# Performance work log

Hardware: AMD Instinct MI355X
Metric: run time of the kernel (lower is better)

Reference implementation:

```python
import jax, jax.numpy as jnp
import numpy as np

T, B_SZ = 1024, 1024
NX, NU, ND, NM, NDT, NH = 128, 64, 32, 32, 32, 128


def setup_inputs() -> dict:
    key = jax.random.key(0)
    ks = jax.random.split(key, 10)
    return {
        "x": jax.random.normal(ks[0], (B_SZ, NX), jnp.float32),
        "M_flow": jax.random.normal(ks[1], (T, B_SZ, NM), jnp.float32),
        "DT": jax.random.normal(ks[2], (T, B_SZ, NDT), jnp.float32),
        "D": jax.random.normal(ks[3], (T, B_SZ, ND), jnp.float32),
        # ConstrainedLinear(nx, nx): weight and scalar init with torch.rand -> uniform[0,1)
        "A_weight": jax.random.uniform(ks[4], (NX, NX), jnp.float32),
        "A_scalar": jax.random.uniform(ks[5], (NX, NX), jnp.float32),
        # nn.Linear(in, out, bias=False) weights are [out, in]
        "B_w": jax.random.normal(ks[6], (NX, NU), jnp.float32) * (1.0 / np.sqrt(NU)),
        "E_w": jax.random.normal(ks[7], (NX, ND), jnp.float32) * (1.0 / np.sqrt(ND)),
        "hf1_w": jax.random.normal(ks[8], (NH, NM + NDT), jnp.float32) * (1.0 / np.sqrt(NM + NDT)),
        "hf2_w": jax.random.normal(ks[9], (NU, NH), jnp.float32) * (1.0 / np.sqrt(NH)),
    }


def reference(x, M_flow, DT, D, A_weight, A_scalar, B_w, E_w, hf1_w, hf2_w):
    # Constrained weight: ((1 - 0.1*sigmoid(scalar)) * softmax(weight, dim=1)).T
    # It is constant across time, so compute once (torch redundantly recomputes it per step).
    s_clamped = 1.0 - 0.1 * jax.nn.sigmoid(A_scalar)
    W_eff = (s_clamped * jax.nn.softmax(A_weight, axis=1)).T  # [nx, nx]

    # Per-step control input u_t depends only on exogenous M_flow/DT -> vectorize over time.
    md = jnp.concatenate([M_flow, DT], axis=2)                # [T, B, n_m+n_dT]
    h = jax.nn.relu(jnp.einsum('tbi,hi->tbh', md, hf1_w))     # [T, B, n_hidden]
    u = jax.nn.relu(jnp.einsum('tbh,uh->tbu', h, hf2_w))      # [T, B, nu]

    # Precompute additive drive B(u_t) + E(d_t); only x@W_eff is sequential.
    drive = jnp.einsum('tbu,xu->tbx', u, B_w) + jnp.einsum('tbd,xd->tbx', D, E_w)

    def step(x_prev, drive_t):
        x_new = x_prev @ W_eff + drive_t
        return x_new, x_new

    _, X = jax.lax.scan(step, x, drive)  # X: [T, B, nx]
    Y = X[:, :, -1]                      # [T, B]
    return X, Y
```

## Files before the change

kernel.cpp:

```cpp
#include <hip/hip_runtime.h>

typedef _Float16 h4 __attribute__((ext_vector_type(4)));
typedef _Float16 h8 __attribute__((ext_vector_type(8)));
typedef __fp16 g2 __attribute__((ext_vector_type(2)));
typedef float f4 __attribute__((ext_vector_type(4)));

#define MFMA16(a, b, c) __builtin_amdgcn_mfma_f32_16x16x32_f16((a), (b), (c), 0, 0, 0)

static constexpr int TT  = 1024;
static constexpr int BS  = 1024;
static constexpr int LCH = 32;
static constexpr int NCH = 32;
static constexpr size_t XTOT = (size_t)TT * BS * 128;

static constexpr size_t WS_WT16 = 0;
static constexpr size_t WS_HF1  = 32768;
static constexpr size_t WS_HF2  = 49152;
static constexpr size_t WS_BW   = 65536;
static constexpr size_t WS_EW   = 81920;
static constexpr size_t WS_W32  = 90112;
static constexpr size_t WS_F    = 131072;
static constexpr size_t WS_INIT = WS_F + (size_t)NCH * BS * 128 * 4;

template <typename T>
__device__ inline T ntload(const T* p) { return __builtin_nontemporal_load(p); }

__device__ inline h4 pk4(f4 a) {
    g2 p0 = __builtin_amdgcn_cvt_pkrtz(a[0], a[1]);
    g2 p1 = __builtin_amdgcn_cvt_pkrtz(a[2], a[3]);
    h4 r;
    r[0] = (_Float16)p0[0]; r[1] = (_Float16)p0[1];
    r[2] = (_Float16)p1[0]; r[3] = (_Float16)p1[1];
    return r;
}
__device__ inline f4 relu4(f4 a) {
    f4 r;
#pragma unroll
    for (int j = 0; j < 4; ++j) r[j] = fmaxf(a[j], 0.f);
    return r;
}

__global__ void prep_kernel(const float* __restrict__ Aw, const float* __restrict__ As,
                            const float* __restrict__ hf1, const float* __restrict__ hf2,
                            const float* __restrict__ Bw, const float* __restrict__ Ew,
                            char* __restrict__ ws)
{
    const int tid = threadIdx.x;
    const int bid = blockIdx.x;
    if (bid < 128) {
        __shared__ float red[128];
        const int n = bid;
        const float a = Aw[n * 128 + tid];
        red[tid] = a;
        __syncthreads();
        for (int s = 64; s > 0; s >>= 1) {
            if (tid < s) red[tid] = fmaxf(red[tid], red[tid + s]);
            __syncthreads();
        }
        const float mx = red[0];
        __syncthreads();
        const float e = expf(a - mx);
        red[tid] = e;
        __syncthreads();
        for (int s = 64; s > 0; s >>= 1) {
            if (tid < s) red[tid] += red[tid + s];
            __syncthreads();
        }
        const float sm  = e / red[0];
        const float asv = As[n * 128 + tid];
        const float sc  = 1.0f - 0.1f * (1.0f / (1.0f + expf(-asv)));
        ((_Float16*)(ws + WS_WT16))[n * 128 + tid] = (_Float16)(sc * sm);
    } else {
        const int b2 = bid - 128;
        for (int i = b2 * 128 + tid; i < 8192; i += 32 * 128) {
            ((_Float16*)(ws + WS_HF1))[i] = (_Float16)hf1[i];
            ((_Float16*)(ws + WS_HF2))[i] = (_Float16)hf2[i];
            ((_Float16*)(ws + WS_BW))[i]  = (_Float16)Bw[i];
            if (i < 4096) ((_Float16*)(ws + WS_EW))[i] = (_Float16)Ew[i];
        }
    }
}

__global__ void w32_kernel(char* __restrict__ ws)
{
    const int tid  = threadIdx.x;
    const int lane = tid & 63;
    const int w    = tid >> 6;
    const int cl   = lane & 15;
    const int gq   = lane >> 4;
    constexpr int LDP = 136;

    __shared__ __align__(16) _Float16 G[2][128 * LDP];
    __shared__ __align__(16) _Float16 H[2][128 * LDP];

    const _Float16* Wt16 = (const _Float16*)(ws + WS_WT16);
    for (int i = tid; i < 2048; i += 256)
        *(h8*)&G[0][(i >> 4) * LDP + (i & 15) * 8] = *(const h8*)&Wt16[i * 8];
    __syncthreads();
    for (int i = tid; i < 16384; i += 256) {
        const int r = i >> 7, cc = i & 127;
        H[0][cc * LDP + r] = G[0][r * LDP + cc];
    }
    __syncthreads();

    int cur = 0;
    for (int s = 0; s < 5; ++s) {
        const _Float16* Gs = G[cur];
        const _Float16* Hs = H[cur];
        _Float16* Gd = G[cur ^ 1];
        _Float16* Hd = H[cur ^ 1];
        f4 aG[8][2], aH[8][2];
#pragma unroll
        for (int mt = 0; mt < 8; ++mt)
#pragma unroll
            for (int nt = 0; nt < 2; ++nt) { aG[mt][nt] = f4{}; aH[mt][nt] = f4{}; }
#pragma unroll
        for (int kk = 0; kk < 4; ++kk) {
            h8 bG0 = *(const h8*)&Hs[((w * 2 + 0) * 16 + cl) * LDP + kk * 32 + gq * 8];
            h8 bG1 = *(const h8*)&Hs[((w * 2 + 1) * 16 + cl) * LDP + kk * 32 + gq * 8];
            h8 bH0 = *(const h8*)&Gs[((w * 2 + 0) * 16 + cl) * LDP + kk * 32 + gq * 8];
            h8 bH1 = *(const h8*)&Gs[((w * 2 + 1) * 16 + cl) * LDP + kk * 32 + gq * 8];
#pragma unroll
            for (int mt = 0; mt < 8; ++mt) {
                h8 ag = *(const h8*)&Gs[(mt * 16 + cl) * LDP + kk * 32 + gq * 8];
                h8 ah = *(const h8*)&Hs[(mt * 16 + cl) * LDP + kk * 32 + gq * 8];
                aG[mt][0] = MFMA16(ag, bG0, aG[mt][0]);
                aG[mt][1] = MFMA16(ag, bG1, aG[mt][1]);
                aH[mt][0] = MFMA16(ah, bH0, aH[mt][0]);
                aH[mt][1] = MFMA16(ah, bH1, aH[mt][1]);
            }
        }
#pragma unroll
        for (int mt = 0; mt < 8; ++mt)
#pragma unroll
            for (int nt = 0; nt < 2; ++nt) {
                h4 hg, hh;
#pragma unroll
                for (int r = 0; r < 4; ++r) {
                    hg[r] = (_Float16)aG[mt][nt][r];
                    hh[r] = (_Float16)aH[mt][nt][r];
                }
                const int col  = (w * 2 + nt) * 16 + cl;
                const int rowb = mt * 16 + gq * 4;
                *(h4*)&Hd[col * LDP + rowb] = hg;
                *(h4*)&Gd[col * LDP + rowb] = hh;
            }
        __syncthreads();
        cur ^= 1;
    }
    _Float16* W32 = (_Float16*)(ws + WS_W32);
    for (int i = tid; i < 2048; i += 256)
        *(h8*)&W32[i * 8] = *(const h8*)&G[cur][(i >> 4) * LDP + (i & 15) * 8];
}

template <bool FINAL>
__global__ __launch_bounds__(256, 1)
void fused_scan(const float* __restrict__ Mfl, const float* __restrict__ DTi,
                const float* __restrict__ Din, char* __restrict__ ws,
                float* __restrict__ Xout, float* __restrict__ Yout)
{
    const int tid  = threadIdx.x;
    const int lane = tid & 63;
    const int w    = tid >> 6;
    const int cl   = lane & 15;
    const int gq   = lane >> 4;
    const int bt   = blockIdx.x & 63;
    const int c    = blockIdx.x >> 6;
    const int b0   = bt * 16;

    const _Float16* Hf1  = (const _Float16*)(ws + WS_HF1);
    const _Float16* Hf2  = (const _Float16*)(ws + WS_HF2);
    const _Float16* Bw16 = (const _Float16*)(ws + WS_BW);
    const _Float16* Ew16 = (const _Float16*)(ws + WS_EW);
    const _Float16* Wt16 = (const _Float16*)(ws + WS_WT16);
    float* Fbuf          = (float*)(ws + WS_F);
    const float* Init    = (const float*)(ws + WS_INIT);

    __shared__ __align__(16) _Float16 mds[4][16 * 64];
    __shared__ __align__(16) _Float16 dts[4][16 * 32];
    __shared__ __align__(16) _Float16 hs[4][16 * 128];
    __shared__ __align__(16) _Float16 us[4][16 * 64];
    __shared__ __align__(16) _Float16 xsh[2][16 * 128];

    h8 hf1f[2][2], bwf[2][2], ewf[2], hf2f[4];
#pragma unroll
    for (int nt = 0; nt < 2; ++nt) {
        const int ng = w * 32 + nt * 16 + cl;
#pragma unroll
        for (int kk = 0; kk < 2; ++kk) {
            hf1f[nt][kk] = *(const h8*)&Hf1[ng * 64 + kk * 32 + gq * 8];
            bwf[nt][kk]  = *(const h8*)&Bw16[ng * 64 + kk * 32 + gq * 8];
        }
        ewf[nt] = *(const h8*)&Ew16[ng * 32 + gq * 8];
    }
    {
        const int ng = w * 16 + cl;
#pragma unroll
        for (int kk = 0; kk < 4; ++kk)
            hf2f[kk] = *(const h8*)&Hf2[ng * 128 + kk * 32 + gq * 8];
    }
    h8 wfp[2][4];
#pragma unroll
    for (int nt = 0; nt < 2; ++nt)
#pragma unroll
        for (int kt = 0; kt < 4; ++kt)
            wfp[nt][kt] =
                *(const h8*)&Wt16[(w * 32 + nt * 16 + cl) * 128 + kt * 32 + gq * 8];

    if constexpr (FINAL) {
        const int row = tid >> 4, c8 = tid & 15;
        const float* src = &Init[((size_t)c * BS + b0 + row) * 128 + c8 * 8];
        f4 v0 = *(const f4*)src, v1 = *(const f4*)(src + 4);
        h8 hv;
#pragma unroll
        for (int j = 0; j < 4; ++j) { hv[j] = (_Float16)v0[j]; hv[4 + j] = (_Float16)v1[j]; }
        *(h8*)&xsh[0][row * 128 + ((c8 ^ row) & 15) * 8] = hv;
    } else {
        h8 z = {};
        *(h8*)&xsh[0][tid * 8] = z;
    }

    const int qrow = (tid & 127) >> 3;
    const int qc4  = (tid & 7) * 4;
    f4 pm[4], pd[4];
    auto GLOAD = [&](int g) {
#pragma unroll
        for (int s = 0; s < 4; ++s) {
            const size_t t  = (size_t)c * LCH + g * 4 + s;
            const size_t rb = (t * BS + b0 + qrow) * 32 + qc4;
            pm[s] = (tid < 128) ? ntload((const f4*)&Mfl[rb]) : ntload((const f4*)&DTi[rb]);
            if (tid < 128) pd[s] = ntload((const f4*)&Din[rb]);
        }
    };
    GLOAD(0);

    _Float16* xcur = xsh[0];
    _Float16* xnxt = xsh[1];

    for (int g = 0; g < 8; ++g) {
#pragma unroll
        for (int s = 0; s < 4; ++s) {
            const int col = (tid < 128) ? qc4 : (32 + qc4);
            h4 hv = pk4(pm[s]);
            *(h4*)&mds[s][qrow * 64 + (((col >> 3) ^ (qrow & 7)) * 8) + (col & 7)] = hv;
            if (tid < 128) {
                h4 h2v = pk4(pd[s]);
                *(h4*)&dts[s][qrow * 32 + (((qc4 >> 3) ^ (qrow & 3)) * 8) + (qc4 & 7)] = h2v;
            }
        }
        if (g < 7) GLOAD(g + 1);
        __syncthreads();

#pragma unroll
        for (int s = 0; s < 4; ++s) {
            f4 ha0 = {}, ha1 = {};
#pragma unroll
            for (int kk = 0; kk < 2; ++kk) {
                h8 a = *(const h8*)&mds[s][cl * 64 + (((kk * 4 + gq) ^ (cl & 7)) * 8)];
                ha0 = MFMA16(hf1f[0][kk], a, ha0);
                ha1 = MFMA16(hf1f[1][kk], a, ha1);
            }
#pragma unroll
            for (int nt = 0; nt < 2; ++nt) {
                const int nb8 = w * 4 + nt * 2 + (gq >> 1);
                h4 hv = pk4(relu4(nt ? ha1 : ha0));
                *(h4*)&hs[s][cl * 128 + ((nb8 ^ cl) & 15) * 8 + (gq & 1) * 4] = hv;
            }
        }
        __syncthreads();

#pragma unroll
        for (int s = 0; s < 4; ++s) {
            f4 ua = {};
#pragma unroll
            for (int kt = 0; kt < 4; ++kt) {
                h8 a = *(const h8*)&hs[s][cl * 128 + (((kt * 4 + gq) ^ cl) & 15) * 8];
                ua = MFMA16(hf2f[kt], a, ua);
            }
            const int ub8 = w * 2 + (gq >> 1);
            h4 uv = pk4(relu4(ua));
            *(h4*)&us[s][cl * 64 + ((ub8 ^ (cl & 7)) & 7) * 8 + (gq & 1) * 4] = uv;
        }
        __syncthreads();

        h4 dv0[4], dv1[4];
#pragma unroll
        for (int s = 0; s < 4; ++s) {
            f4 a20 = {}, a21 = {};
#pragma unroll
            for (int kk = 0; kk < 2; ++kk) {
                h8 a = *(const h8*)&us[s][cl * 64 + (((kk * 4 + gq) ^ (cl & 7)) & 7) * 8];
                a20 = MFMA16(bwf[0][kk], a, a20);
                a21 = MFMA16(bwf[1][kk], a, a21);
            }
            {
                h8 ad = *(const h8*)&dts[s][cl * 32 + ((gq ^ (cl & 3)) * 8)];
                a20 = MFMA16(ewf[0], ad, a20);
                a21 = MFMA16(ewf[1], ad, a21);
            }
            dv0[s] = pk4(a20);
            dv1[s] = pk4(a21);
        }

#pragma unroll
        for (int s = 0; s < 4; ++s) {
            h8 xf[4];
#pragma unroll
            for (int kt = 0; kt < 4; ++kt)
                xf[kt] = *(const h8*)&xcur[cl * 128 + (((kt * 4 + gq) ^ cl) & 15) * 8];
            f4 acc0, acc1;
#pragma unroll
            for (int r = 0; r < 4; ++r) {
                acc0[r] = (float)dv0[s][r];
                acc1[r] = (float)dv1[s][r];
            }
#pragma unroll
            for (int kt = 0; kt < 4; ++kt) {
                acc0 = MFMA16(wfp[0][kt], xf[kt], acc0);
                acc1 = MFMA16(wfp[1][kt], xf[kt], acc1);
            }

            if constexpr (FINAL) {
                const size_t t = (size_t)c * LCH + g * 4 + s;
                float* xp = &Xout[(t * BS + b0 + cl) * 128 + w * 32 + gq * 4];
                __builtin_nontemporal_store(acc0, (f4*)xp);
                __builtin_nontemporal_store(acc1, (f4*)(xp + 16));
                if (w == 3 && gq == 3)
                    __builtin_nontemporal_store(acc1[3], &Yout[t * BS + b0 + cl]);
            }
            const bool last = (g == 7) && (s == 3);
            if (!FINAL && last) {
                float* fp = &Fbuf[((size_t)c * BS + b0 + cl) * 128 + w * 32 + gq * 4];
                *(f4*)fp = acc0;
                *(f4*)(fp + 16) = acc1;
            }
            if (!last) {
#pragma unroll
                for (int nt = 0; nt < 2; ++nt) {
                    h4 hv;
#pragma unroll
                    for (int r = 0; r < 4; ++r) hv[r] = (_Float16)(nt ? acc1[r] : acc0[r]);
                    const int nb8 = w * 4 + nt * 2 + (gq >> 1);
                    *(h4*)&xnxt[cl * 128 + ((nb8 ^ cl) & 15) * 8 + (gq & 1) * 4] = hv;
                }
                __syncthreads();
                _Float16* tmp = xcur; xcur = xnxt; xnxt = tmp;
            }
        }
    }
}

__global__ __launch_bounds__(64, 1)
void carry_kernel(const float* __restrict__ x0, char* __restrict__ ws, int n_steps)
{
    const int lane = threadIdx.x;
    const int cl = lane & 15, gq = lane >> 4;
    const int b0 = blockIdx.x * 16;

    const _Float16* W32 = (const _Float16*)(ws + WS_W32);
    const float* Fbuf   = (const float*)(ws + WS_F);
    float* Init         = (float*)(ws + WS_INIT);

    __shared__ __align__(16) _Float16 tbuf[16 * 128];

    h8 wf[8][4];
#pragma unroll
    for (int nt = 0; nt < 8; ++nt)
#pragma unroll
        for (int kt = 0; kt < 4; ++kt)
            wf[nt][kt] = *(const h8*)&W32[(nt * 16 + cl) * 128 + kt * 32 + gq * 8];

    h8 xf[4];
    {
        f4 iv[8];
#pragma unroll
        for (int nt = 0; nt < 8; ++nt)
            iv[nt] = *(const f4*)&x0[(size_t)(b0 + cl) * 128 + nt * 16 + gq * 4];
#pragma unroll
        for (int nt = 0; nt < 8; ++nt)
            *(f4*)&Init[(size_t)(b0 + cl) * 128 + nt * 16 + gq * 4] = iv[nt];
#pragma unroll
        for (int nt = 0; nt < 8; ++nt) {
            h4 hv;
#pragma unroll
            for (int r = 0; r < 4; ++r) hv[r] = (_Float16)iv[nt][r];
            *(h4*)&tbuf[cl * 128 + (((nt * 2 + (gq >> 1)) ^ cl) & 15) * 8 + (gq & 1) * 4] = hv;
        }
#pragma unroll
        for (int kt = 0; kt < 4; ++kt)
            xf[kt] = *(const h8*)&tbuf[cl * 128 + (((kt * 4 + gq) ^ cl) & 15) * 8];
    }

    for (int cc = 1; cc <= n_steps; ++cc) {
        f4 acc[8];
#pragma unroll
        for (int nt = 0; nt < 8; ++nt)
            acc[nt] = *(const f4*)&Fbuf[((size_t)(cc - 1) * BS + b0 + cl) * 128 + nt * 16 + gq * 4];
#pragma unroll
        for (int kt = 0; kt < 4; ++kt)
#pragma unroll
            for (int nt = 0; nt < 8; ++nt)
                acc[nt] = MFMA16(wf[nt][kt], xf[kt], acc[nt]);
#pragma unroll
        for (int nt = 0; nt < 8; ++nt)
            *(f4*)&Init[((size_t)cc * BS + b0 + cl) * 128 + nt * 16 + gq * 4] = acc[nt];
        if (cc < n_steps) {
#pragma unroll
            for (int nt = 0; nt < 8; ++nt) {
                h4 hv;
#pragma unroll
                for (int r = 0; r < 4; ++r) hv[r] = (_Float16)acc[nt][r];
                *(h4*)&tbuf[cl * 128 + (((nt * 2 + (gq >> 1)) ^ cl) & 15) * 8 + (gq & 1) * 4] = hv;
            }
#pragma unroll
            for (int kt = 0; kt < 4; ++kt)
                xf[kt] = *(const h8*)&tbuf[cl * 128 + (((kt * 4 + gq) ^ cl) & 15) * 8];
        }
    }
}

extern "C" void kernel_launch(void* const* d_in, const int* in_sizes, int n_in,
                              void* d_out, int out_size, void* d_ws, size_t ws_size,
                              hipStream_t stream)
{
    const float* x_in = (const float*)d_in[0];
    const float* Mfl  = (const float*)d_in[1];
    const float* DTi  = (const float*)d_in[2];
    const float* Din  = (const float*)d_in[3];
    const float* Aw   = (const float*)d_in[4];
    const float* As   = (const float*)d_in[5];
    const float* Bw   = (const float*)d_in[6];
    const float* Ew   = (const float*)d_in[7];
    const float* hf1  = (const float*)d_in[8];
    const float* hf2  = (const float*)d_in[9];
    char* ws    = (char*)d_ws;
    float* Xout = (float*)d_out;
    float* Yout = Xout + XTOT;

    prep_kernel<<<dim3(160), dim3(128), 0, stream>>>(Aw, As, hf1, hf2, Bw, Ew, ws);
    w32_kernel<<<dim3(1), dim3(256), 0, stream>>>(ws);

    fused_scan<false><<<dim3(31 * 64), dim3(256), 0, stream>>>(Mfl, DTi, Din, ws,
                                                               nullptr, nullptr);
    carry_kernel<<<dim3(64), dim3(64), 0, stream>>>(x_in, ws, 31);
    fused_scan<true><<<dim3(32 * 64), dim3(256), 0, stream>>>(Mfl, DTi, Din, ws,
                                                              Xout, Yout);
}
```

Baseline: 426.5 us.

## Replace two-pass chunked scan with local scan plus power-matrix correction pass

Instead of rerunning the full MLP+scan pass a second time with carried initial states, the first pass now stores zero-initialised local states in fp16, and a new correction kernel adds W^k applied to each chunk's initial state. Powers W^1..W^16 are built by repeated squaring and products. Chunk length drops from 32 to 64 chunks of 16 steps, and the carry kernel uses W^16 with 63 sequential steps. This avoids recomputing the MLP and drive, at the cost of an extra fp16 intermediate buffer write and read, extra setup kernels, and possible accuracy loss from fp16 storage.

```diff
diff --git a/kernel.cpp b/kernel.cpp
--- a/kernel.cpp
+++ b/kernel.cpp
@@ -9,8 +9,8 @@
 
 static constexpr int TT  = 1024;
 static constexpr int BS  = 1024;
-static constexpr int LCH = 32;
-static constexpr int NCH = 32;
+static constexpr int LCH = 16;
+static constexpr int NCH = 64;
 static constexpr size_t XTOT = (size_t)TT * BS * 128;
 
 static constexpr size_t WS_WT16 = 0;
@@ -18,9 +18,11 @@
 static constexpr size_t WS_HF2  = 49152;
 static constexpr size_t WS_BW   = 65536;
 static constexpr size_t WS_EW   = 81920;
-static constexpr size_t WS_W32  = 90112;
-static constexpr size_t WS_F    = 131072;
+static constexpr size_t WS_FACT = 90112;
+static constexpr size_t WS_POW  = 352256;
+static constexpr size_t WS_F    = 876544;
 static constexpr size_t WS_INIT = WS_F + (size_t)NCH * BS * 128 * 4;
+static constexpr size_t WS_XL   = WS_INIT + (size_t)NCH * BS * 128 * 4;
 
 template <typename T>
 __device__ inline T ntload(const T* p) { return __builtin_nontemporal_load(p); }
@@ -81,7 +83,7 @@
     }
 }
 
-__global__ void w32_kernel(char* __restrict__ ws)
+__global__ void sq_kernel(char* __restrict__ ws)
 {
     const int tid  = threadIdx.x;
     const int lane = tid & 63;
@@ -94,17 +96,24 @@
     __shared__ __align__(16) _Float16 H[2][128 * LDP];
 
     const _Float16* Wt16 = (const _Float16*)(ws + WS_WT16);
-    for (int i = tid; i < 2048; i += 256)
-        *(h8*)&G[0][(i >> 4) * LDP + (i & 15) * 8] = *(const h8*)&Wt16[i * 8];
+    _Float16* FACT       = (_Float16*)(ws + WS_FACT);
+
+    for (int i = tid; i < 2048; i += 256) {
+        h8 v = *(const h8*)&Wt16[i * 8];
+        *(h8*)&G[0][(i >> 4) * LDP + (i & 15) * 8] = v;
+        *(h8*)&FACT[i * 8] = v;
+    }
     __syncthreads();
     for (int i = tid; i < 16384; i += 256) {
         const int r = i >> 7, cc = i & 127;
         H[0][cc * LDP + r] = G[0][r * LDP + cc];
     }
     __syncthreads();
+    for (int i = tid; i < 2048; i += 256)
+        *(h8*)&FACT[16384 + i * 8] = *(const h8*)&H[0][(i >> 4) * LDP + (i & 15) * 8];
 
     int cur = 0;
-    for (int s = 0; s < 5; ++s) {
+    for (int s = 0; s < 3; ++s) {
         const _Float16* Gs = G[cur];
         const _Float16* Hs = H[cur];
         _Float16* Gd = G[cur ^ 1];
@@ -130,6 +139,7 @@
                 aH[mt][1] = MFMA16(ah, bH1, aH[mt][1]);
             }
         }
+        __syncthreads();
 #pragma unroll
         for (int mt = 0; mt < 8; ++mt)
 #pragma unroll
@@ -147,17 +157,111 @@
             }
         __syncthreads();
         cur ^= 1;
-    }
-    _Float16* W32 = (_Float16*)(ws + WS_W32);
+        const size_t toff = (size_t)(2 * (s + 1)) * 16384;
+        for (int i = tid; i < 2048; i += 256) {
+            *(h8*)&FACT[toff + i * 8] =
+                *(const h8*)&G[cur][(i >> 4) * LDP + (i & 15) * 8];
+            *(h8*)&FACT[toff + 16384 + i * 8] =
+                *(const h8*)&H[cur][(i >> 4) * LDP + (i & 15) * 8];
+        }
+        __syncthreads();
+    }
+}
+
+__global__ void prod_kernel(char* __restrict__ ws)
+{
+    const int tid  = threadIdx.x;
+    const int lane = tid & 63;
+    const int w    = tid >> 6;
+    const int cl   = lane & 15;
+    const int gq   = lane >> 4;
+    const int p    = blockIdx.x + 1;
+    constexpr int LDP = 136;
+
+    const _Float16* FACT = (const _Float16*)(ws + WS_FACT);
+    _Float16* POW        = (_Float16*)(ws + WS_POW);
+
+    int fl[4], nf = 0;
+    if (p == 16) { fl[0] = 8; fl[1] = 8; nf = 2; }
+    else { for (int b = 8; b >= 1; b >>= 1) if (p & b) fl[nf++] = b; }
+
+    if (nf == 1) {
+        const int fi = (p == 1) ? 0 : (p == 2) ? 1 : (p == 4) ? 2 : 3;
+        for (int i = tid; i < 2048; i += 256)
+            *(h8*)&POW[(size_t)(p - 1) * 16384 + i * 8] =
+                *(const h8*)&FACT[(size_t)(2 * fi) * 16384 + i * 8];
+        return;
+    }
+
+    __shared__ __align__(16) _Float16 TA[128 * LDP], UA[128 * LDP];
+    __shared__ __align__(16) _Float16 TB[128 * LDP], UB[128 * LDP];
+
+    auto fidx = [](int f) { return (f == 1) ? 0 : (f == 2) ? 1 : (f == 4) ? 2 : 3; };
+    auto loadpair = [&](int f, _Float16* T, _Float16* U) {
+        const size_t toff = (size_t)(2 * fidx(f)) * 16384;
+        for (int i = tid; i < 2048; i += 256) {
+            *(h8*)&T[(i >> 4) * LDP + (i & 15) * 8] = *(const h8*)&FACT[toff + i * 8];
+            *(h8*)&U[(i >> 4) * LDP + (i & 15) * 8] =
+                *(const h8*)&FACT[toff + 16384 + i * 8];
+        }
+    };
+
+    loadpair(fl[0], TA, UA);
+    _Float16 *Tc = TA, *Uc = UA, *To = TB, *Uo = UB;
+
+    for (int j = 1; j < nf; ++j) {
+        loadpair(fl[j], To, Uo);
+        __syncthreads();
+        f4 aA[8][2], aB[8][2];
+#pragma unroll
+        for (int mt = 0; mt < 8; ++mt)
+#pragma unroll
+            for (int nt = 0; nt < 2; ++nt) { aA[mt][nt] = f4{}; aB[mt][nt] = f4{}; }
+#pragma unroll
+        for (int kk = 0; kk < 4; ++kk) {
+            h8 bA0 = *(const h8*)&Uc[((w * 2 + 0) * 16 + cl) * LDP + kk * 32 + gq * 8];
+            h8 bA1 = *(const h8*)&Uc[((w * 2 + 1) * 16 + cl) * LDP + kk * 32 + gq * 8];
+            h8 bB0 = *(const h8*)&To[((w * 2 + 0) * 16 + cl) * LDP + kk * 32 + gq * 8];
+            h8 bB1 = *(const h8*)&To[((w * 2 + 1) * 16 + cl) * LDP + kk * 32 + gq * 8];
+#pragma unroll
+            for (int mt = 0; mt < 8; ++mt) {
+                h8 aT = *(const h8*)&To[(mt * 16 + cl) * LDP + kk * 32 + gq * 8];
+                h8 aU = *(const h8*)&Uc[(mt * 16 + cl) * LDP + kk * 32 + gq * 8];
+                aA[mt][0] = MFMA16(aT, bA0, aA[mt][0]);
+                aA[mt][1] = MFMA16(aT, bA1, aA[mt][1]);
+                aB[mt][0] = MFMA16(aU, bB0, aB[mt][0]);
+                aB[mt][1] = MFMA16(aU, bB1, aB[mt][1]);
+            }
+        }
+        __syncthreads();
+#pragma unroll
+        for (int mt = 0; mt < 8; ++mt)
+#pragma unroll
+            for (int nt = 0; nt < 2; ++nt) {
+                h4 hA, hB;
+#pragma unroll
+                for (int r = 0; r < 4; ++r) {
+                    hA[r] = (_Float16)aA[mt][nt][r];
+                    hB[r] = (_Float16)aB[mt][nt][r];
+                }
+                const int col  = (w * 2 + nt) * 16 + cl;
+                const int rowb = mt * 16 + gq * 4;
+                *(h4*)&Uo[col * LDP + rowb] = hA;
+                *(h4*)&To[col * LDP + rowb] = hB;
+            }
+        __syncthreads();
+        _Float16* t;
+        t = Tc; Tc = To; To = t;
+        t = Uc; Uc = Uo; Uo = t;
+    }
     for (int i = tid; i < 2048; i += 256)
-        *(h8*)&W32[i * 8] = *(const h8*)&G[cur][(i >> 4) * LDP + (i & 15) * 8];
-}
-
-template <bool FINAL>
+        *(h8*)&POW[(size_t)(p - 1) * 16384 + i * 8] =
+            *(const h8*)&Tc[(i >> 4) * LDP + (i & 15) * 8];
+}
+
 __global__ __launch_bounds__(256, 1)
-void fused_scan(const float* __restrict__ Mfl, const float* __restrict__ DTi,
-                const float* __restrict__ Din, char* __restrict__ ws,
-                float* __restrict__ Xout, float* __restrict__ Yout)
+void fused_local(const float* __restrict__ Mfl, const float* __restrict__ DTi,
+                 const float* __restrict__ Din, char* __restrict__ ws)
 {
     const int tid  = threadIdx.x;
     const int lane = tid & 63;
@@ -174,7 +278,7 @@
     const _Float16* Ew16 = (const _Float16*)(ws + WS_EW);
     const _Float16* Wt16 = (const _Float16*)(ws + WS_WT16);
     float* Fbuf          = (float*)(ws + WS_F);
-    const float* Init    = (const float*)(ws + WS_INIT);
+    _Float16* XL         = (_Float16*)(ws + WS_XL);
 
     __shared__ __align__(16) _Float16 mds[4][16 * 64];
     __shared__ __align__(16) _Float16 dts[4][16 * 32];
@@ -207,15 +311,7 @@
             wfp[nt][kt] =
                 *(const h8*)&Wt16[(w * 32 + nt * 16 + cl) * 128 + kt * 32 + gq * 8];
 
-    if constexpr (FINAL) {
-        const int row = tid >> 4, c8 = tid & 15;
-        const float* src = &Init[((size_t)c * BS + b0 + row) * 128 + c8 * 8];
-        f4 v0 = *(const f4*)src, v1 = *(const f4*)(src + 4);
-        h8 hv;
-#pragma unroll
-        for (int j = 0; j < 4; ++j) { hv[j] = (_Float16)v0[j]; hv[4 + j] = (_Float16)v1[j]; }
-        *(h8*)&xsh[0][row * 128 + ((c8 ^ row) & 15) * 8] = hv;
-    } else {
+    {
         h8 z = {};
         *(h8*)&xsh[0][tid * 8] = z;
     }
@@ -237,7 +333,7 @@
     _Float16* xcur = xsh[0];
     _Float16* xnxt = xsh[1];
 
-    for (int g = 0; g < 8; ++g) {
+    for (int g = 0; g < 4; ++g) {
 #pragma unroll
         for (int s = 0; s < 4; ++s) {
             const int col = (tid < 128) ? qc4 : (32 + qc4);
@@ -248,7 +344,7 @@
                 *(h4*)&dts[s][qrow * 32 + (((qc4 >> 3) ^ (qrow & 3)) * 8) + (qc4 & 7)] = h2v;
             }
         }
-        if (g < 7) GLOAD(g + 1);
+        if (g < 3) GLOAD(g + 1);
         __syncthreads();
 
 #pragma unroll
@@ -320,21 +416,23 @@
                 acc1 = MFMA16(wfp[1][kt], xf[kt], acc1);
             }
 
-            if constexpr (FINAL) {
+            {
                 const size_t t = (size_t)c * LCH + g * 4 + s;
-                float* xp = &Xout[(t * BS + b0 + cl) * 128 + w * 32 + gq * 4];
-                __builtin_nontemporal_store(acc0, (f4*)xp);
-                __builtin_nontemporal_store(acc1, (f4*)(xp + 16));
-                if (w == 3 && gq == 3)
-                    __builtin_nontemporal_store(acc1[3], &Yout[t * BS + b0 + cl]);
-            }
-            const bool last = (g == 7) && (s == 3);
-            if (!FINAL && last) {
+                h8 o;
+#pragma unroll
+                for (int r = 0; r < 4; ++r) {
+                    o[r]     = (_Float16)acc0[r];
+                    o[4 + r] = (_Float16)acc1[r];
+                }
+                *(h8*)&XL[((t * 64 + bt) * 256 + tid) * 8] = o;
+            }
+
+            const bool last = (g == 3) && (s == 3);
+            if (last) {
                 float* fp = &Fbuf[((size_t)c * BS + b0 + cl) * 128 + w * 32 + gq * 4];
                 *(f4*)fp = acc0;
                 *(f4*)(fp + 16) = acc1;
-            }
-            if (!last) {
+            } else {
 #pragma unroll
                 for (int nt = 0; nt < 2; ++nt) {
                     h4 hv;
@@ -351,13 +449,13 @@
 }
 
 __global__ __launch_bounds__(64, 1)
-void carry_kernel(const float* __restrict__ x0, char* __restrict__ ws, int n_steps)
+void carry_kernel(const float* __restrict__ x0, char* __restrict__ ws)
 {
     const int lane = threadIdx.x;
     const int cl = lane & 15, gq = lane >> 4;
     const int b0 = blockIdx.x * 16;
 
-    const _Float16* W32 = (const _Float16*)(ws + WS_W32);
+    const _Float16* W16 = (const _Float16*)(ws + WS_POW) + (size_t)15 * 16384;
     const float* Fbuf   = (const float*)(ws + WS_F);
     float* Init         = (float*)(ws + WS_INIT);
 
@@ -368,7 +466,7 @@
     for (int nt = 0; nt < 8; ++nt)
 #pragma unroll
         for (int kt = 0; kt < 4; ++kt)
-            wf[nt][kt] = *(const h8*)&W32[(nt * 16 + cl) * 128 + kt * 32 + gq * 8];
+            wf[nt][kt] = *(const h8*)&W16[(nt * 16 + cl) * 128 + kt * 32 + gq * 8];
 
     h8 xf[4];
     {
@@ -391,7 +489,7 @@
             xf[kt] = *(const h8*)&tbuf[cl * 128 + (((kt * 4 + gq) ^ cl) & 15) * 8];
     }
 
-    for (int cc = 1; cc <= n_steps; ++cc) {
+    for (int cc = 1; cc < NCH; ++cc) {
         f4 acc[8];
 #pragma unroll
         for (int nt = 0; nt < 8; ++nt)
@@ -404,7 +502,7 @@
 #pragma unroll
         for (int nt = 0; nt < 8; ++nt)
             *(f4*)&Init[((size_t)cc * BS + b0 + cl) * 128 + nt * 16 + gq * 4] = acc[nt];
-        if (cc < n_steps) {
+        if (cc < NCH - 1) {
 #pragma unroll
             for (int nt = 0; nt < 8; ++nt) {
                 h4 hv;
@@ -417,6 +515,79 @@
                 xf[kt] = *(const h8*)&tbuf[cl * 128 + (((kt * 4 + gq) ^ cl) & 15) * 8];
         }
     }
+}
+
+__global__ __launch_bounds__(256, 1)
+void correct_kernel(char* __restrict__ ws, float* __restrict__ Xout,
+                    float* __restrict__ Yout)
+{
+    const int tid  = threadIdx.x;
+    const int lane = tid & 63;
+    const int w    = tid >> 6;
+    const int cl   = lane & 15;
+    const int gq   = lane >> 4;
+    const int k    = blockIdx.x >> 6;
+    const int bt   = blockIdx.x & 63;
+    const int b0   = bt * 16;
+
+    const _Float16* Tk  = (const _Float16*)(ws + WS_POW) + (size_t)k * 16384;
+    const float* Init   = (const float*)(ws + WS_INIT);
+    const _Float16* XL  = (const _Float16*)(ws + WS_XL);
+
+    h8 wfp[2][4];
+#pragma unroll
+    for (int nt = 0; nt < 2; ++nt)
+#pragma unroll
+        for (int kt = 0; kt < 4; ++kt)
+            wfp[nt][kt] =
+                *(const h8*)&Tk[(w * 32 + nt * 16 + cl) * 128 + kt * 32 + gq * 8];
+
+    auto LOADC = [&](int c, h8* xf, h8& xl) {
+        const float* ib = &Init[((size_t)c * BS + b0 + cl) * 128 + gq * 8];
+#pragma unroll
+        for (int kt = 0; kt < 4; ++kt) {
+            f4 v0 = *(const f4*)&ib[kt * 32];
+            f4 v1 = *(const f4*)&ib[kt * 32 + 4];
+            h8 x;
+#pragma unroll
+            for (int r = 0; r < 4; ++r) {
+                x[r]     = (_Float16)v0[r];
+                x[4 + r] = (_Float16)v1[r];
+            }
+            xf[kt] = x;
+        }
+        const size_t t = (size_t)c * LCH + k;
+        xl = *(const h8*)&XL[((t * 64 + bt) * 256 + tid) * 8];
+    };
+
+#define CSTEP(C, XF, XLR)                                                            \
+    {                                                                                \
+        f4 acc0, acc1;                                                               \
+        _Pragma("unroll") for (int r = 0; r < 4; ++r) {                              \
+            acc0[r] = (float)XLR[r];                                                 \
+            acc1[r] = (float)XLR[4 + r];                                             \
+        }                                                                            \
+        _Pragma("unroll") for (int kt = 0; kt < 4; ++kt) {                           \
+            acc0 = MFMA16(wfp[0][kt], XF[kt], acc0);                                 \
+            acc1 = MFMA16(wfp[1][kt], XF[kt], acc1);                                 \
+        }                                                                            \
+        if ((C) + 2 < NCH) LOADC((C) + 2, XF, XLR);                                  \
+        const size_t t = (size_t)(C) * LCH + k;                                      \
+        float* xp = &Xout[(t * BS + b0 + cl) * 128 + w * 32 + gq * 4];               \
+        __builtin_nontemporal_store(acc0, (f4*)xp);                                  \
+        __builtin_nontemporal_store(acc1, (f4*)(xp + 16));                           \
+        if (w == 3 && gq == 3)                                                       \
+            __builtin_nontemporal_store(acc1[3], &Yout[t * BS + b0 + cl]);           \
+    }
+
+    h8 xfA[4], xfB[4], xlA, xlB;
+    LOADC(0, xfA, xlA);
+    LOADC(1, xfB, xlB);
+    for (int c = 0; c < NCH; c += 2) {
+        CSTEP(c, xfA, xlA);
+        CSTEP(c + 1, xfB, xlB);
+    }
+#undef CSTEP
 }
 
 extern "C" void kernel_launch(void* const* d_in, const int* in_sizes, int n_in,
@@ -438,11 +609,10 @@
     float* Yout = Xout + XTOT;
 
     prep_kernel<<<dim3(160), dim3(128), 0, stream>>>(Aw, As, hf1, hf2, Bw, Ew, ws);
-    w32_kernel<<<dim3(1), dim3(256), 0, stream>>>(ws);
-
-    fused_scan<false><<<dim3(31 * 64), dim3(256), 0, stream>>>(Mfl, DTi, Din, ws,
-                                                               nullptr, nullptr);
-    carry_kernel<<<dim3(64), dim3(64), 0, stream>>>(x_in, ws, 31);
-    fused_scan<true><<<dim3(32 * 64), dim3(256), 0, stream>>>(Mfl, DTi, Din, ws,
-                                                              Xout, Yout);
-}
+    sq_kernel<<<dim3(1), dim3(256), 0, stream>>>(ws);
+    prod_kernel<<<dim3(16), dim3(256), 0, stream>>>(ws);
+
+    fused_local<<<dim3(NCH * 64), dim3(256), 0, stream>>>(Mfl, DTi, Din, ws);
+    carry_kernel<<<dim3(64), dim3(64), 0, stream>>>(x_in, ws);
+    correct_kernel<<<dim3(16 * 64), dim3(256), 0, stream>>>(ws, Xout, Yout);
+}
```

New measurement: 724.6 us. 69.9% more time.
